# Kernel optimization log

Measured on AMD Instinct MI355X. Metric: run time of the kernel, lower is better.

The kernel has to match this reference:

```python
import jax, jax.numpy as jnp
import numpy as np
import math

EMB_DIM = 1024
NUM_HEADS = 16
D_H = EMB_DIM // NUM_HEADS
B, S = 2, 2048


def setup_inputs() -> dict:
    key = jax.random.key(0)
    ks = jax.random.split(key, 6)
    limit = math.sqrt(6.0 / (EMB_DIM + D_H))  # xavier_uniform per head
    x = jax.random.normal(ks[0], (B, S, EMB_DIM), dtype=jnp.float32)
    Wq = jax.random.uniform(ks[1], (NUM_HEADS, EMB_DIM, D_H), jnp.float32, -limit, limit)
    Wk = jax.random.uniform(ks[2], (NUM_HEADS, EMB_DIM, D_H), jnp.float32, -limit, limit)
    Wv = jax.random.uniform(ks[3], (NUM_HEADS, EMB_DIM, D_H), jnp.float32, -limit, limit)
    bq = jnp.zeros((NUM_HEADS, D_H), jnp.float32)
    bk = jnp.zeros((NUM_HEADS, D_H), jnp.float32)
    bv = jnp.zeros((NUM_HEADS, D_H), jnp.float32)
    limo = math.sqrt(6.0 / (EMB_DIM + EMB_DIM))
    W_O = jax.random.uniform(ks[4], (EMB_DIM, EMB_DIM), jnp.float32, -limo, limo)
    causal_mask = jnp.tril(jnp.ones((S, S), jnp.float32))
    padding_mask = jnp.zeros((B, S), jnp.bool_)  # all-False: nothing padded
    return {"x": x, "Wq": Wq, "bq": bq, "Wk": Wk, "bk": bk, "Wv": Wv,
            "bv": bv, "W_O": W_O, "causal_mask": causal_mask,
            "padding_mask": padding_mask}


def reference(x, Wq, bq, Wk, bk, Wv, bv, W_O, causal_mask, padding_mask):
    # Per-head projections, vectorized over heads: [B,S,E] x [H,E,D] -> [B,H,S,D]
    Q = jnp.einsum('bse,hed->bhsd', x, Wq) + bq[None, :, None, :]
    K = jnp.einsum('bse,hed->bhsd', x, Wk) + bk[None, :, None, :]
    V = jnp.einsum('bse,hed->bhsd', x, Wv) + bv[None, :, None, :]
    scores = jnp.einsum('bhsd,bhtd->bhst', Q, K) / math.sqrt(D_H)
    neg_inf = jnp.float32(-jnp.inf)
    scores = jnp.where(causal_mask[None, None, :, :] == 0, neg_inf, scores)
    scores = jnp.where(padding_mask[:, None, None, :], neg_inf, scores)
    attn = jax.nn.softmax(scores, axis=-1)
    out = jnp.einsum('bhst,bhtd->bhsd', attn, V)  # [B,H,S,D]
    # concat heads in order (dim=-1) -> [B,S,H*D]
    x_concat = out.transpose(0, 2, 1, 3).reshape(B, S, EMB_DIM)
    return x_concat @ W_O
```

## Files before the change

kernel.cpp:

```cpp
#include <hip/hip_runtime.h>
#include <hip/hip_bf16.h>


typedef __hip_bfloat16 bf16;
typedef __attribute__((ext_vector_type(8))) short bfrag;
typedef __attribute__((ext_vector_type(4))) float f32x4;
typedef __attribute__((ext_vector_type(16))) float f32x16;
typedef __attribute__((ext_vector_type(4))) short short4v;

#define MFMA16(a, b, c) __builtin_amdgcn_mfma_f32_16x16x32_bf16(a, b, c, 0, 0, 0)
#define MFMA32(a, b, c) __builtin_amdgcn_mfma_f32_32x32x16_bf16(a, b, c, 0, 0, 0)

__device__ __forceinline__ unsigned pk2(float a, float b) {
  union { __hip_bfloat162 h; unsigned u; } w;
  w.h = __float22bfloat162_rn(make_float2(a, b));
  return w.u;
}

__device__ __forceinline__ void gload16(const bf16* g, bf16* l) {
  __builtin_amdgcn_global_load_lds(
      (const __attribute__((address_space(1))) void*)(g),
      (__attribute__((address_space(3))) void*)(l), 16, 0, 0);
}

__device__ __forceinline__ void barrier_raw() {
  asm volatile("" ::: "memory");
  __builtin_amdgcn_s_barrier();
  asm volatile("" ::: "memory");
}

__device__ __forceinline__ void barrier_lgkm() {
  asm volatile("s_waitcnt lgkmcnt(0)" ::: "memory");
  __builtin_amdgcn_s_barrier();
  asm volatile("" ::: "memory");
}

__global__ __launch_bounds__(256) void prep_all(const float* __restrict__ x,
                                                const float* __restrict__ Wq,
                                                const float* __restrict__ Wk,
                                                const float* __restrict__ Wv,
                                                const float* __restrict__ Wo,
                                                bf16* __restrict__ xb,
                                                bf16* __restrict__ WqkvT,
                                                bf16* __restrict__ WoT) {
  __shared__ bf16 tile[64][80];
  int id = blockIdx.x;
  int t = threadIdx.x;
  if (id < 2048) {
    int i = id * 2048 + t * 8;
    float4 a = *(const float4*)(x + i);
    float4 b = *(const float4*)(x + i + 4);
    union { bf16 h[8]; bfrag v; } tmp;
    tmp.h[0] = __float2bfloat16(a.x); tmp.h[1] = __float2bfloat16(a.y);
    tmp.h[2] = __float2bfloat16(a.z); tmp.h[3] = __float2bfloat16(a.w);
    tmp.h[4] = __float2bfloat16(b.x); tmp.h[5] = __float2bfloat16(b.y);
    tmp.h[6] = __float2bfloat16(b.z); tmp.h[7] = __float2bfloat16(b.w);
    *(bfrag*)(xb + i) = tmp.v;
    return;
  }
  int wid = id - 2048;
  const float* src;
  bf16* dst;
  int srcld, dstld, r0, c0;
  if (wid < 768) {
    int w = wid >> 8, h = (wid >> 4) & 15;
    r0 = (wid & 15) * 64; c0 = 0;
    src = ((w == 0) ? Wq : (w == 1) ? Wk : Wv) + (long)h * 1024 * 64;
    dst = WqkvT + ((long)w * 1024 + h * 64) * 1024;
    srcld = 64; dstld = 1024;
  } else {
    int j = wid - 768;
    c0 = (j & 15) * 64; r0 = (j >> 4) * 64;
    src = Wo; dst = WoT;
    srcld = 1024; dstld = 1024;
  }
  int lr = t >> 3, lc = (t & 7) << 3;
#pragma unroll
  for (int p = 0; p < 2; ++p) {
    int r = lr + p * 32;
    const float* s = src + (long)(r0 + r) * srcld + c0 + lc;
    union { bf16 h8[8]; bfrag v; } tmp;
#pragma unroll
    for (int j = 0; j < 8; ++j) tmp.h8[j] = __float2bfloat16(s[j]);
    *(bfrag*)(&tile[r][lc]) = tmp.v;
  }
  __syncthreads();
#pragma unroll
  for (int p = 0; p < 2; ++p) {
    int c = lr + p * 32;
    union { bf16 h8[8]; bfrag v; } tmp;
#pragma unroll
    for (int j = 0; j < 8; ++j) tmp.h8[j] = tile[lc + j][c];
    *(bfrag*)(dst + (long)(c0 + c) * dstld + r0 + lc) = tmp.v;
  }
}

__global__ __launch_bounds__(512, 2) void gemm_qkv128(const bf16* __restrict__ xb,
                                                      const bf16* __restrict__ WT,
                                                      const float* __restrict__ bq,
                                                      const float* __restrict__ bk,
                                                      const float* __restrict__ bv,
                                                      bf16* __restrict__ Q,
                                                      bf16* __restrict__ K_,
                                                      bf16* __restrict__ Vt) {
  extern __shared__ bf16 lds[];
  int id = blockIdx.x;
  int xcd = id & 7, idx = id >> 3;
  int tile = xcd * 32 + idx;
  int mt = tile & 15, nt = tile >> 4;
  int m0 = mt * 256, n0 = nt * 192;

  int t = threadIdx.x;
  int wave = t >> 6, lane = t & 63, quad = lane >> 4, col = lane & 15;
  int wm = wave >> 2, wn = wave & 3;

  int schunk = 8 * ((t & 7) ^ ((t >> 3) & 7));
  const bf16* aSrc = xb + (long)(m0 + (t >> 3)) * 1024 + schunk;
  const bf16* bSrc = WT + (long)(n0 + (t >> 3)) * 1024 + schunk;
  int wv512 = wave * 512;

  int xoff0 = (quad * 8) ^ ((col & 7) << 3);
  const bf16* aRdB = lds + wm * 8192 + col * 64;
  const bf16* bRdB = lds + 32768 + (wn * 48 + col) * 64;

  f32x4 acc[8][3] = {};

#define STA(BUF, HALF, G, KS)                                                  \
  gload16(aSrc + (long)((HALF)*128 + (G)*64) * 1024 + (KS)*64,                 \
          lds + (BUF)*16384 + (HALF)*8192 + (G)*4096 + wv512)
#define STB(BUF, G, KS)                                                        \
  gload16(bSrc + (long)((G)*64) * 1024 + (KS)*64,                              \
          lds + 32768 + (BUF)*12288 + (G)*4096 + wv512)

#define PHASE(BUF, MH, KC, STAGES, VMW)                                        \
  {                                                                            \
    int xk = xoff0 ^ ((KC)*32);                                                \
    bfrag ra[4], rb[3];                                                        \
    _Pragma("unroll") for (int u = 0; u < 4; ++u)                              \
      ra[u] = *(const bfrag*)(aRdB + (BUF)*16384 + (MH)*4096 + u * 1024 + xk); \
    _Pragma("unroll") for (int c2 = 0; c2 < 3; ++c2)                           \
      rb[c2] = *(const bfrag*)(bRdB + (BUF)*12288 + c2 * 1024 + xk);           \
    STAGES;                                                                    \
    VMW;                                                                       \
    barrier_raw();                                                             \
    __builtin_amdgcn_s_setprio(1);                                             \
    _Pragma("unroll") for (int ni = 0; ni < 3; ++ni)                           \
      _Pragma("unroll") for (int mi2 = 0; mi2 < 4; ++mi2)                      \
        acc[(MH)*4 + mi2][ni] = MFMA16(ra[mi2], rb[ni], acc[(MH)*4 + mi2][ni]);\
    __builtin_amdgcn_s_setprio(0);                                             \
    barrier_raw();                                                             \
  }

#define VM2 asm volatile("s_waitcnt vmcnt(2)" ::: "memory")
#define NOVM

  STA(0, 0, 0, 0); STA(0, 1, 0, 0); STA(0, 0, 1, 0); STA(0, 1, 1, 0);
  STB(0, 0, 0); STB(0, 1, 0); STB(0, 2, 0);
  STA(1, 0, 0, 1); STA(1, 1, 0, 1);
  VM2;
  barrier_raw();

  for (int it = 0; it < 8; ++it) {
    int ksB = 2 * it + 1;
    int kA  = (it < 7) ? 2 * it + 2 : 14;
    int ksB2 = (it < 7) ? 2 * it + 3 : 15;
    PHASE(0, 0, 0, { STA(1, 0, 1, ksB); STA(1, 1, 1, ksB); }, NOVM);
    PHASE(0, 0, 1, { STB(1, 0, ksB); STB(1, 1, ksB); }, NOVM);
    PHASE(0, 1, 0, { STB(1, 2, ksB); }, NOVM);
    PHASE(0, 1, 1, { STA(0, 0, 0, kA); STA(0, 1, 0, kA); }, VM2);
    PHASE(1, 0, 0, { STA(0, 0, 1, kA); STA(0, 1, 1, kA); }, NOVM);
    PHASE(1, 0, 1, { STB(0, 0, kA); STB(0, 1, kA); }, NOVM);
    PHASE(1, 1, 0, { STB(0, 2, kA); }, NOVM);
    PHASE(1, 1, 1, { STA(1, 0, 0, ksB2); STA(1, 1, 0, ksB2); }, VM2);
  }
#undef PHASE
#undef STA
#undef STB
#undef VM2
#undef NOVM

  asm volatile("s_waitcnt vmcnt(0)" ::: "memory");
  barrier_raw();

  const float SC2 = 0.18033688f;
  int b = m0 >> 11, sbase = m0 & 2047;

  if (n0 < 1920) {
#pragma unroll
    for (int ni = 0; ni < 3; ++ni) {
      int n = wn * 48 + ni * 16 + col;
      int ng = n0 + n;
      int s01 = ng >> 10;
      float bvv = s01 ? bk[ng & 1023] : bq[ng & 1023];
      float qsv = s01 ? 1.0f : SC2;
#pragma unroll
      for (int mi = 0; mi < 8; ++mi) {
        int mrow = wm * 128 + mi * 16 + quad * 4;
#pragma unroll
        for (int r = 0; r < 4; ++r)
          lds[(mrow + r) * 200 + n] = __float2bfloat16((acc[mi][ni][r] + bvv) * qsv);
      }
    }
    barrier_raw();
    int row = t >> 1, half = t & 1;
#pragma unroll
    for (int s = 0; s < 12; ++s) {
      int cl = 96 * half + 8 * s;
      int ng = n0 + cl;
      int s01 = ng >> 10, within = ng & 1023;
      int h = within >> 6, d = within & 63;
      bf16* dst = s01 ? K_ : Q;
      *(bfrag*)(dst + ((long)((b << 4) + h) * 2048 + sbase + row) * 64 + d) =
          *(const bfrag*)(lds + row * 200 + cl);
    }
  } else if (n0 == 1920) {
#pragma unroll
    for (int ni = 0; ni < 3; ++ni) {
      int n = wn * 48 + ni * 16 + col;
      int ng = n0 + n;
      if (ng < 2048) {
        float bvv = bk[ng & 1023];
#pragma unroll
        for (int mi = 0; mi < 8; ++mi) {
          int mrow = wm * 128 + mi * 16 + quad * 4;
#pragma unroll
          for (int r = 0; r < 4; ++r)
            lds[(mrow + r) * 136 + n] = __float2bfloat16(acc[mi][ni][r] + bvv);
        }
      } else {
        int vn = n - 128;
        float bvv = bv[ng & 1023];
#pragma unroll
        for (int mi = 0; mi < 8; ++mi) {
          int m = wm * 128 + mi * 16 + quad * 4;
          union { unsigned u[2]; unsigned long long ull; } pkd;
          pkd.u[0] = pk2(acc[mi][ni][0] + bvv, acc[mi][ni][1] + bvv);
          pkd.u[1] = pk2(acc[mi][ni][2] + bvv, acc[mi][ni][3] + bvv);
          *(unsigned long long*)(lds + 34816 + vn * 264 + m) = pkd.ull;
        }
      }
    }
    barrier_raw();
#pragma unroll
    for (int p = 0; p < 8; ++p) {
      int u = p * 512 + t;
      int row = u >> 4, cl = (u & 15) * 8;
      int within = (n0 + cl) & 1023;
      int h = within >> 6, d = within & 63;
      *(bfrag*)(K_ + ((long)((b << 4) + h) * 2048 + sbase + row) * 64 + d) =
          *(const bfrag*)(lds + row * 136 + cl);
    }
#pragma unroll
    for (int p = 0; p < 4; ++p) {
      int u = p * 512 + t;
      int vn = u >> 5, seg = (u & 31) * 8;
      int within = (n0 + 128 + vn) & 1023;
      int h = within >> 6, d = within & 63;
      *(bfrag*)(Vt + ((long)((b << 4) + h) * 64 + d) * 2048 + sbase + seg) =
          *(const bfrag*)(lds + 34816 + vn * 264 + seg);
    }
  } else {
#pragma unroll
    for (int ni = 0; ni < 3; ++ni) {
      int n = wn * 48 + ni * 16 + col;
      int ng = n0 + n;
      float bvv = bv[ng & 1023];
#pragma unroll
      for (int mi = 0; mi < 8; ++mi) {
        int m = wm * 128 + mi * 16 + quad * 4;
        union { unsigned u[2]; unsigned long long ull; } pkd;
        pkd.u[0] = pk2(acc[mi][ni][0] + bvv, acc[mi][ni][1] + bvv);
        pkd.u[1] = pk2(acc[mi][ni][2] + bvv, acc[mi][ni][3] + bvv);
        *(unsigned long long*)(lds + n * 264 + m) = pkd.ull;
      }
    }
    barrier_raw();
#pragma unroll
    for (int p = 0; p < 12; ++p) {
      int u = p * 512 + t;
      int rn = u >> 5, seg = (u & 31) * 8;
      int within = (n0 + rn) & 1023;
      int h = within >> 6, d = within & 63;
      *(bfrag*)(Vt + ((long)((b << 4) + h) * 64 + d) * 2048 + sbase + seg) =
          *(const bfrag*)(lds + rn * 264 + seg);
    }
  }
}

__global__ __launch_bounds__(256) void gemm_out(const bf16* __restrict__ O,
                                                const bf16* __restrict__ Bt,
                                                float* __restrict__ Cf) {
  const int K = 1024;
  __shared__ bf16 As[2][128 * 64];
  __shared__ bf16 Bs[2][64 * 64];
  int id = blockIdx.x;
  int xcd = id & 7, sw = id >> 3;
  int m0 = ((xcd << 2) | (sw & 3)) * 128;
  int n0 = (sw >> 2) * 64;
  int t = threadIdx.x;
  int wave = t >> 6, lane = t & 63, quad = lane >> 4, col = lane & 15;
  int wr = (wave >> 1) * 64, wc = (wave & 1) * 32;
  f32x4 acc[2][4] = {};

  int schunk = 8 * ((t & 7) ^ ((t >> 3) & 7));
  int ob = m0 >> 11;
  const bf16* AsrcB = O + (long)ob * 2097152 + (long)((m0 & 2047) + (t >> 3)) * 64 + schunk;
  const bf16* BsrcB = Bt + (long)(n0 + (t >> 3)) * K + schunk;
  int wv = wave * 512;
  int xoff0 = (quad * 8) ^ ((col & 7) << 3);

#define OUT_STAGE(bi, k0n)                                                 \
  {                                                                        \
    long ko = ((long)((k0n) >> 6)) * 131072;                               \
    _Pragma("unroll") for (int i = 0; i < 4; ++i)                          \
      gload16(AsrcB + ko + (long)(32 * i) * 64, &As[bi][i * 2048 + wv]);   \
    _Pragma("unroll") for (int i = 0; i < 2; ++i)                          \
      gload16(BsrcB + (k0n) + (long)(32 * i) * K, &Bs[bi][i * 2048 + wv]); \
  }

  OUT_STAGE(0, 0);
  __syncthreads();
  for (int k0 = 0; k0 < K; k0 += 64) {
    int cur = (k0 >> 6) & 1;
    if (k0 + 64 < K) OUT_STAGE(cur ^ 1, k0 + 64);
#pragma unroll
    for (int kc = 0; kc < 2; ++kc) {
      int xk = xoff0 ^ (kc * 32);
      bfrag ra[4], rb[2];
#pragma unroll
      for (int i = 0; i < 4; ++i)
        ra[i] = *(const bfrag*)(&As[cur][(wr + 16 * i + col) * 64 + xk]);
#pragma unroll
      for (int c = 0; c < 2; ++c)
        rb[c] = *(const bfrag*)(&Bs[cur][(wc + 16 * c + col) * 64 + xk]);
#pragma unroll
      for (int c = 0; c < 2; ++c)
#pragma unroll
        for (int i = 0; i < 4; ++i) acc[c][i] = MFMA16(ra[i], rb[c], acc[c][i]);
    }
    __syncthreads();
  }
#undef OUT_STAGE

#pragma unroll
  for (int c = 0; c < 2; ++c) {
    int n = n0 + wc + 16 * c + col;
#pragma unroll
    for (int i = 0; i < 4; ++i)
#pragma unroll
      for (int r = 0; r < 4; ++r) {
        int m = m0 + wr + 16 * i + quad * 4 + r;
        Cf[(long)m * 1024 + n] = acc[c][i][r];
      }
  }
}

__global__ __launch_bounds__(256) void attn_kernel(const bf16* __restrict__ Q,
                                                   const bf16* __restrict__ K_,
                                                   const bf16* __restrict__ Vt,
                                                   bf16* __restrict__ O) {
  int id = blockIdx.x;
  int xcd = id & 7, jj = id >> 3;
  int qt = 31 - (jj >> 2);
  int bh = ((jj & 3) << 3) | xcd;

  __shared__ bf16 Ks[128][72];
  __shared__ bf16 Vs[64][136];

  int t = threadIdx.x, wave = t >> 6, lane = t & 63;
  int qh = wave >> 1, jh = wave & 1, hi = lane >> 5, l5 = lane & 31;

  int krow = t >> 3, kg = (t & 7) * 8;
  int vrow = t >> 4, vg = (t & 15) * 8;
  const bf16* KuBase = K_ + (long)bh * 2048 * 64;
  const bf16* VuBase = Vt + (long)bh * 64 * 2048;
  int kL = krow * 64 + kg;
  int vL = vrow * 2048 + vg;

  int q0 = qt * 64;
  int nj = (qt >> 1) + 1;
  int qi = q0 + 32 * qh + l5;

  bfrag qa[4];
  const bf16* qp = Q + ((long)bh * 2048 + q0 + 32 * qh + l5) * 64 + hi * 8;
#pragma unroll
  for (int kd = 0; kd < 4; ++kd) qa[kd] = *(const bfrag*)(qp + kd * 16);

  f32x16 o0, o1;
  float lsum = 0.f;
#pragma unroll
  for (int r = 0; r < 16; ++r) { o0[r] = 0.f; o1[r] = 0.f; }

  bfrag kreg[4], vreg[4];
#pragma unroll
  for (int i = 0; i < 4; ++i) {
    kreg[i] = *(const bfrag*)(KuBase + kL + i * 2048);
    vreg[i] = *(const bfrag*)(VuBase + vL + i * 32768);
  }

  for (int jt = 0; jt < nj; ++jt) {
    int j0 = jt * 128;
    barrier_lgkm();
#pragma unroll
    for (int i = 0; i < 4; ++i) {
      *(bfrag*)(&Ks[krow + 32 * i][kg]) = kreg[i];
      *(bfrag*)(&Vs[vrow + 16 * i][vg]) = vreg[i];
    }
    int jn = (jt + 1 < nj) ? j0 + 128 : j0;
    const bf16* kp = KuBase + (long)jn * 64;
    const bf16* vp = VuBase + jn;
#pragma unroll
    for (int i = 0; i < 4; ++i) {
      kreg[i] = *(const bfrag*)(kp + kL + i * 2048);
      vreg[i] = *(const bfrag*)(vp + vL + i * 32768);
    }
    barrier_lgkm();

    bool lastT = (jt == nj - 1);
    if (lastT && jh == 1 && ((qt & 1) == 0)) continue;

    f32x16 s0, s1;
#pragma unroll
    for (int r = 0; r < 16; ++r) { s0[r] = 0.f; s1[r] = 0.f; }
    __builtin_amdgcn_s_setprio(1);
#pragma unroll
    for (int kd = 0; kd < 4; ++kd) {
      bfrag ka0 = *(const bfrag*)(&Ks[jh * 64 + l5][kd * 16 + hi * 8]);
      bfrag ka1 = *(const bfrag*)(&Ks[jh * 64 + 32 + l5][kd * 16 + hi * 8]);
      s0 = MFMA32(ka0, qa[kd], s0);
      s1 = MFMA32(ka1, qa[kd], s1);
    }
    __builtin_amdgcn_s_setprio(0);

    unsigned g[2][4][2];
#pragma unroll
    for (int jb = 0; jb < 2; ++jb) {
      float pv[16];
      float ls = 0.f;
#pragma unroll
      for (int r = 0; r < 16; ++r) {
        int jl = (r & 3) + 8 * (r >> 2) + 4 * hi;
        int j = j0 + jh * 64 + jb * 32 + jl;
        float sv = jb ? s1[r] : s0[r];
        float p = __builtin_amdgcn_exp2f(sv);
        if (lastT) p = (j <= qi) ? p : 0.f;
        ls += p;
        pv[r] = p;
      }
      lsum += ls;
#pragma unroll
      for (int gg = 0; gg < 4; ++gg) {
        g[jb][gg][0] = pk2(pv[4 * gg], pv[4 * gg + 1]);
        g[jb][gg][1] = pk2(pv[4 * gg + 2], pv[4 * gg + 3]);
      }
    }

    __builtin_amdgcn_s_setprio(1);
#pragma unroll
    for (int jb = 0; jb < 2; ++jb) {
#pragma unroll
      for (int c = 0; c < 2; ++c) {
        unsigned a0 = g[jb][2 * c][0], a1 = g[jb][2 * c][1];
        unsigned b0 = g[jb][2 * c + 1][0], b1 = g[jb][2 * c + 1][1];
        asm("v_permlane32_swap_b32 %0, %1" : "+v"(a0), "+v"(b0));
        asm("v_permlane32_swap_b32 %0, %1" : "+v"(a1), "+v"(b1));
        union { unsigned u[4]; bfrag f; } pf;
        pf.u[0] = a0;
        pf.u[1] = a1;
        pf.u[2] = b0;
        pf.u[3] = b1;
        int kk = jh * 64 + jb * 32 + c * 16 + hi * 8;
        bfrag av0 = *(const bfrag*)(&Vs[l5][kk]);
        bfrag av1 = *(const bfrag*)(&Vs[32 + l5][kk]);
        o0 = MFMA32(av0, pf.f, o0);
        o1 = MFMA32(av1, pf.f, o1);
      }
    }
    __builtin_amdgcn_s_setprio(0);
  }

  lsum += __shfl_xor(lsum, 32, 64);

  __syncthreads();
  float* Osc = (float*)&Ks[0][0];
  float* Lsc = (float*)&Vs[0][0];
  bf16* Of = (bf16*)((char*)&Vs[0][0] + 512);
  int q = 32 * qh + l5;
  if (jh == 1) {
#pragma unroll
    for (int r = 0; r < 16; ++r) {
      int d = (r & 3) + 8 * (r >> 2) + 4 * hi;
      Osc[q * 68 + d] = o0[r];
      Osc[q * 68 + 32 + d] = o1[r];
    }
    if (hi == 0) Lsc[q] = lsum;
  }
  __syncthreads();
  if (jh == 0) {
    float inv = 1.f / (lsum + Lsc[q]);
#pragma unroll
    for (int r = 0; r < 16; ++r) {
      int d = (r & 3) + 8 * (r >> 2) + 4 * hi;
      Of[q * 72 + d] = __float2bfloat16((o0[r] + Osc[q * 68 + d]) * inv);
      Of[q * 72 + 32 + d] = __float2bfloat16((o1[r] + Osc[q * 68 + 32 + d]) * inv);
    }
  }
  __syncthreads();
  int row = t >> 2, off = (t & 3) * 16;
  bf16* po = O + ((long)bh * 2048 + q0 + row) * 64 + off;
  *(bfrag*)(po) = *(const bfrag*)(&Of[row * 72 + off]);
  *(bfrag*)(po + 8) = *(const bfrag*)(&Of[row * 72 + off + 8]);
}

extern "C" void kernel_launch(void* const* d_in, const int* in_sizes, int n_in,
                              void* d_out, int out_size, void* d_ws, size_t ws_size,
                              hipStream_t stream) {
  const float* x  = (const float*)d_in[0];
  const float* Wq = (const float*)d_in[1];
  const float* bq = (const float*)d_in[2];
  const float* Wk = (const float*)d_in[3];
  const float* bk = (const float*)d_in[4];
  const float* Wv = (const float*)d_in[5];
  const float* bv = (const float*)d_in[6];
  const float* Wo = (const float*)d_in[7];
  float* out = (float*)d_out;

  bf16* ws = (bf16*)d_ws;
  const long MB1 = 1 << 20;
  bf16* WqkvT = ws + 0 * MB1;
  bf16* WoT   = ws + 3 * MB1;
  bf16* Q     = ws + 4 * MB1;
  bf16* K_    = ws + 8 * MB1;
  bf16* Vt    = ws + 12 * MB1;
  bf16* O     = ws + 16 * MB1;
  bf16* xb    = ws + 20 * MB1;

  prep_all<<<3072, 256, 0, stream>>>(x, Wq, Wk, Wv, Wo, xb, WqkvT, WoT);
  gemm_qkv128<<<256, 512, 114688, stream>>>(xb, WqkvT, bq, bk, bv, Q, K_, Vt);
  attn_kernel<<<1024, 256, 0, stream>>>(Q, K_, Vt, O);
  gemm_out<<<512, 256, 0, stream>>>(O, WoT, out);
}
```

Measured before the change: 187.6 us.

## Load K fragments directly to registers and double-buffer V in LDS

The attention kernel no longer stages K through shared memory. Each wave loads its K MFMA fragments straight from global memory into registers and prefetches the next tile's fragments while the current tile is being computed. V is double-buffered in LDS, so only one barrier per iteration is needed instead of two. This is meant to cut LDS traffic and barrier stalls. In exchange it raises register pressure and makes each wave load K redundantly from global or L2.

```diff
diff --git a/kernel.cpp b/kernel.cpp
--- a/kernel.cpp
+++ b/kernel.cpp
@@ -364,18 +364,16 @@
   int qt = 31 - (jj >> 2);
   int bh = ((jj & 3) << 3) | xcd;
 
-  __shared__ bf16 Ks[128][72];
-  __shared__ bf16 Vs[64][136];
+  __shared__ bf16 Vs[2][64][136];
 
   int t = threadIdx.x, wave = t >> 6, lane = t & 63;
   int qh = wave >> 1, jh = wave & 1, hi = lane >> 5, l5 = lane & 31;
 
-  int krow = t >> 3, kg = (t & 7) * 8;
   int vrow = t >> 4, vg = (t & 15) * 8;
-  const bf16* KuBase = K_ + (long)bh * 2048 * 64;
   const bf16* VuBase = Vt + (long)bh * 64 * 2048;
-  int kL = krow * 64 + kg;
   int vL = vrow * 2048 + vg;
+
+  const bf16* Kfb = K_ + ((long)bh * 2048 + jh * 64 + l5) * 64 + hi * 8;
 
   int q0 = qt * 64;
   int nj = (qt >> 1) + 1;
@@ -391,100 +389,119 @@
 #pragma unroll
   for (int r = 0; r < 16; ++r) { o0[r] = 0.f; o1[r] = 0.f; }
 
-  bfrag kreg[4], vreg[4];
-#pragma unroll
-  for (int i = 0; i < 4; ++i) {
-    kreg[i] = *(const bfrag*)(KuBase + kL + i * 2048);
-    vreg[i] = *(const bfrag*)(VuBase + vL + i * 32768);
-  }
+  bfrag kc0[4], kc1[4];
+#pragma unroll
+  for (int kd = 0; kd < 4; ++kd) {
+    kc0[kd] = *(const bfrag*)(Kfb + kd * 16);
+    kc1[kd] = *(const bfrag*)(Kfb + 2048 + kd * 16);
+  }
+  {
+    bfrag v0[4];
+#pragma unroll
+    for (int i = 0; i < 4; ++i) v0[i] = *(const bfrag*)(VuBase + vL + i * 32768);
+#pragma unroll
+    for (int i = 0; i < 4; ++i) *(bfrag*)(&Vs[0][vrow + 16 * i][vg]) = v0[i];
+  }
+  __syncthreads();
 
   for (int jt = 0; jt < nj; ++jt) {
     int j0 = jt * 128;
+    int jn = (jt + 1 < nj) ? j0 + 128 : j0;
+    int cur = jt & 1, nxt = cur ^ 1;
+
+    bfrag vregN[4];
+    {
+      const bf16* vp = VuBase + jn;
+#pragma unroll
+      for (int i = 0; i < 4; ++i) vregN[i] = *(const bfrag*)(vp + vL + i * 32768);
+    }
+
+    bool lastT = (jt == nj - 1);
+    bool skip = lastT && (jh == 1) && ((qt & 1) == 0);
+    bfrag kn0[4], kn1[4];
+
+    if (!skip) {
+      f32x16 s0, s1;
+#pragma unroll
+      for (int r = 0; r < 16; ++r) { s0[r] = 0.f; s1[r] = 0.f; }
+      __builtin_amdgcn_s_setprio(1);
+#pragma unroll
+      for (int kd = 0; kd < 4; ++kd) {
+        s0 = MFMA32(kc0[kd], qa[kd], s0);
+        s1 = MFMA32(kc1[kd], qa[kd], s1);
+      }
+      __builtin_amdgcn_s_setprio(0);
+
+      {
+        const bf16* kpn = Kfb + (long)jn * 64;
+#pragma unroll
+        for (int kd = 0; kd < 4; ++kd) {
+          kn0[kd] = *(const bfrag*)(kpn + kd * 16);
+          kn1[kd] = *(const bfrag*)(kpn + 2048 + kd * 16);
+        }
+      }
+
+      unsigned g[2][4][2];
+#pragma unroll
+      for (int jb = 0; jb < 2; ++jb) {
+        float pv[16];
+        float ls = 0.f;
+#pragma unroll
+        for (int r = 0; r < 16; ++r) {
+          int jl = (r & 3) + 8 * (r >> 2) + 4 * hi;
+          int j = j0 + jh * 64 + jb * 32 + jl;
+          float sv = jb ? s1[r] : s0[r];
+          float p = __builtin_amdgcn_exp2f(sv);
+          if (lastT) p = (j <= qi) ? p : 0.f;
+          ls += p;
+          pv[r] = p;
+        }
+        lsum += ls;
+#pragma unroll
+        for (int gg = 0; gg < 4; ++gg) {
+          g[jb][gg][0] = pk2(pv[4 * gg], pv[4 * gg + 1]);
+          g[jb][gg][1] = pk2(pv[4 * gg + 2], pv[4 * gg + 3]);
+        }
+      }
+
+      __builtin_amdgcn_s_setprio(1);
+#pragma unroll
+      for (int jb = 0; jb < 2; ++jb) {
+#pragma unroll
+        for (int c = 0; c < 2; ++c) {
+          unsigned a0 = g[jb][2 * c][0], a1 = g[jb][2 * c][1];
+          unsigned b0 = g[jb][2 * c + 1][0], b1 = g[jb][2 * c + 1][1];
+          asm("v_permlane32_swap_b32 %0, %1" : "+v"(a0), "+v"(b0));
+          asm("v_permlane32_swap_b32 %0, %1" : "+v"(a1), "+v"(b1));
+          union { unsigned u[4]; bfrag f; } pf;
+          pf.u[0] = a0;
+          pf.u[1] = a1;
+          pf.u[2] = b0;
+          pf.u[3] = b1;
+          int kk = jh * 64 + jb * 32 + c * 16 + hi * 8;
+          bfrag av0 = *(const bfrag*)(&Vs[cur][l5][kk]);
+          bfrag av1 = *(const bfrag*)(&Vs[cur][32 + l5][kk]);
+          o0 = MFMA32(av0, pf.f, o0);
+          o1 = MFMA32(av1, pf.f, o1);
+        }
+      }
+      __builtin_amdgcn_s_setprio(0);
+    }
+
+#pragma unroll
+    for (int i = 0; i < 4; ++i) *(bfrag*)(&Vs[nxt][vrow + 16 * i][vg]) = vregN[i];
+#pragma unroll
+    for (int kd = 0; kd < 4; ++kd) { kc0[kd] = kn0[kd]; kc1[kd] = kn1[kd]; }
+
     barrier_lgkm();
-#pragma unroll
-    for (int i = 0; i < 4; ++i) {
-      *(bfrag*)(&Ks[krow + 32 * i][kg]) = kreg[i];
-      *(bfrag*)(&Vs[vrow + 16 * i][vg]) = vreg[i];
-    }
-    int jn = (jt + 1 < nj) ? j0 + 128 : j0;
-    const bf16* kp = KuBase + (long)jn * 64;
-    const bf16* vp = VuBase + jn;
-#pragma unroll
-    for (int i = 0; i < 4; ++i) {
-      kreg[i] = *(const bfrag*)(kp + kL + i * 2048);
-      vreg[i] = *(const bfrag*)(vp + vL + i * 32768);
-    }
-    barrier_lgkm();
-
-    bool lastT = (jt == nj - 1);
-    if (lastT && jh == 1 && ((qt & 1) == 0)) continue;
-
-    f32x16 s0, s1;
-#pragma unroll
-    for (int r = 0; r < 16; ++r) { s0[r] = 0.f; s1[r] = 0.f; }
-    __builtin_amdgcn_s_setprio(1);
-#pragma unroll
-    for (int kd = 0; kd < 4; ++kd) {
-      bfrag ka0 = *(const bfrag*)(&Ks[jh * 64 + l5][kd * 16 + hi * 8]);
-      bfrag ka1 = *(const bfrag*)(&Ks[jh * 64 + 32 + l5][kd * 16 + hi * 8]);
-      s0 = MFMA32(ka0, qa[kd], s0);
-      s1 = MFMA32(ka1, qa[kd], s1);
-    }
-    __builtin_amdgcn_s_setprio(0);
-
-    unsigned g[2][4][2];
-#pragma unroll
-    for (int jb = 0; jb < 2; ++jb) {
-      float pv[16];
-      float ls = 0.f;
-#pragma unroll
-      for (int r = 0; r < 16; ++r) {
-        int jl = (r & 3) + 8 * (r >> 2) + 4 * hi;
-        int j = j0 + jh * 64 + jb * 32 + jl;
-        float sv = jb ? s1[r] : s0[r];
-        float p = __builtin_amdgcn_exp2f(sv);
-        if (lastT) p = (j <= qi) ? p : 0.f;
-        ls += p;
-        pv[r] = p;
-      }
-      lsum += ls;
-#pragma unroll
-      for (int gg = 0; gg < 4; ++gg) {
-        g[jb][gg][0] = pk2(pv[4 * gg], pv[4 * gg + 1]);
-        g[jb][gg][1] = pk2(pv[4 * gg + 2], pv[4 * gg + 3]);
-      }
-    }
-
-    __builtin_amdgcn_s_setprio(1);
-#pragma unroll
-    for (int jb = 0; jb < 2; ++jb) {
-#pragma unroll
-      for (int c = 0; c < 2; ++c) {
-        unsigned a0 = g[jb][2 * c][0], a1 = g[jb][2 * c][1];
-        unsigned b0 = g[jb][2 * c + 1][0], b1 = g[jb][2 * c + 1][1];
-        asm("v_permlane32_swap_b32 %0, %1" : "+v"(a0), "+v"(b0));
-        asm("v_permlane32_swap_b32 %0, %1" : "+v"(a1), "+v"(b1));
-        union { unsigned u[4]; bfrag f; } pf;
-        pf.u[0] = a0;
-        pf.u[1] = a1;
-        pf.u[2] = b0;
-        pf.u[3] = b1;
-        int kk = jh * 64 + jb * 32 + c * 16 + hi * 8;
-        bfrag av0 = *(const bfrag*)(&Vs[l5][kk]);
-        bfrag av1 = *(const bfrag*)(&Vs[32 + l5][kk]);
-        o0 = MFMA32(av0, pf.f, o0);
-        o1 = MFMA32(av1, pf.f, o1);
-      }
-    }
-    __builtin_amdgcn_s_setprio(0);
   }
 
   lsum += __shfl_xor(lsum, 32, 64);
 
   __syncthreads();
-  float* Osc = (float*)&Ks[0][0];
-  float* Lsc = (float*)&Vs[0][0];
-  bf16* Of = (bf16*)((char*)&Vs[0][0] + 512);
+  float* Osc = (float*)&Vs[0][0][0];
+  float* Lsc = (float*)((char*)&Vs[0][0][0] + 17408);
+  bf16* Of = (bf16*)((char*)&Vs[0][0][0] + 17664);
   int q = 32 * qh + l5;
   if (jh == 1) {
 #pragma unroll
```

Result: slower. 201.2 us (+7.3%).
